# Optimization experiments

Hardware: AMD Instinct MI355X
Metric: run time of the kernel (lower is better)

The kernel has to match this reference:

```python
import jax, jax.numpy as jnp
import numpy as np

TOPK = 32  # init kwarg topk=32, method='softmax'


def setup_inputs() -> dict:
    key = jax.random.key(0)
    k1, k2 = jax.random.split(key)
    X1 = jax.random.normal(k1, (8192, 64), dtype=jnp.float32)
    X2 = jax.random.normal(k2, (8192, 64), dtype=jnp.float32)
    return {"X1": X1, "X2": X2}


def reference(X1, X2):
    # pairwise Euclidean distance via the matmul expansion (same math as torch.cdist p=2)
    sq = (
        jnp.sum(X1 * X1, axis=-1)[:, None]
        + jnp.sum(X2 * X2, axis=-1)[None, :]
        - 2.0 * (X1 @ X2.T)
    )  # [N1, N2]
    neg_dist = -jnp.sqrt(jnp.maximum(sq, 0.0))
    # top-k along dim=1, softmax over the k selected values
    val, idx = jax.lax.top_k(neg_dist, TOPK)          # [N1, K]
    score = jax.nn.softmax(val, axis=1)               # [N1, K]
    # scatter scores back into a dense zero matrix
    rows = jnp.arange(neg_dist.shape[0])[:, None]     # [N1, 1]
    out = jnp.zeros_like(neg_dist).at[rows, idx].set(score)
    return out, score
```

## Files before the change

### kernel.cpp

```cpp
#include <hip/hip_runtime.h>
#include <math.h>
#include <float.h>
#include <limits.h>

#define N 8192
#define D 64
#define TOPK 32
#define TILE 128
#define CAP 1024
#define CAP2 256
#define MARGIN 1.0f

typedef _Float16 f16x8 __attribute__((ext_vector_type(8)));
typedef _Float16 f16x4v __attribute__((ext_vector_type(4)));
typedef __attribute__((ext_vector_type(4))) float f32x4;

__device__ __forceinline__ unsigned ford(float f) {
    unsigned u = __float_as_uint(f);
    return u ^ ((u & 0x80000000u) ? 0xFFFFFFFFu : 0x80000000u);
}
__device__ __forceinline__ float finv(unsigned u) {
    unsigned b = (u & 0x80000000u) ? (u ^ 0x80000000u) : ~u;
    return __uint_as_float(b);
}

__global__ __launch_bounds__(256) void prep_kernel(
    const float* __restrict__ X1, const float* __restrict__ X2,
    float* __restrict__ nrm,
    _Float16* __restrict__ X1f, _Float16* __restrict__ X2f)
{
    int id = blockIdx.x * blockDim.x + threadIdx.x;
    if (id >= 2 * N) return;
    const float* X = (id < N) ? X1 : X2;
    _Float16* H = (id < N) ? X1f : X2f;
    int r = (id < N) ? id : id - N;
    const float4* p = (const float4*)(X + (size_t)r * D);
    f16x4v* ph = (f16x4v*)(H + (size_t)r * D);
    float s = 0.f;
#pragma unroll
    for (int q = 0; q < D / 4; ++q) {
        float4 v = p[q];
        s += v.x * v.x + v.y * v.y + v.z * v.z + v.w * v.w;
        f16x4v h;
        h[0] = (_Float16)v.x; h[1] = (_Float16)v.y;
        h[2] = (_Float16)v.z; h[3] = (_Float16)v.w;
        ph[q] = h;
    }
    nrm[id] = s;
}

#define MFMA16F(a, b, c) __builtin_amdgcn_mfma_f32_16x16x32_f16((a), (b), (c), 0, 0, 0)

__device__ __forceinline__ void stage_tile(
    const _Float16* __restrict__ gsrc, _Float16* __restrict__ lds, int t)
{
    const f16x8* g = (const f16x8*)gsrc;
#pragma unroll
    for (int it = 0; it < 4; ++it) {
        int idx = it * 256 + t;
        int row = idx >> 3;
        int co  = (idx & 7) << 3;
        int sw  = co ^ ((row & 7) << 3);
        *(f16x8*)&lds[row * 64 + sw] = g[idx];
    }
}

__device__ __forceinline__ void mfma_core_lds(
    const _Float16* __restrict__ Asm, const _Float16* __restrict__ Bsm,
    int wr, int wc, int lane, f32x4 acc[4][4])
{
    const int l15 = lane & 15;
    const int lg8 = (lane >> 4) * 8;

    f16x8 ah[4][2];
#pragma unroll
    for (int mt = 0; mt < 4; ++mt) {
        int row = wr * 64 + mt * 16 + l15;
        int sw0 = (lg8)      ^ ((row & 7) << 3);
        int sw1 = (32 + lg8) ^ ((row & 7) << 3);
        ah[mt][0] = *(const f16x8*)&Asm[row * 64 + sw0];
        ah[mt][1] = *(const f16x8*)&Asm[row * 64 + sw1];
    }
#pragma unroll
    for (int nt = 0; nt < 4; ++nt) {
        int row = wc * 64 + nt * 16 + l15;
        int sw0 = (lg8)      ^ ((row & 7) << 3);
        int sw1 = (32 + lg8) ^ ((row & 7) << 3);
        f16x8 b0 = *(const f16x8*)&Bsm[row * 64 + sw0];
        f16x8 b1 = *(const f16x8*)&Bsm[row * 64 + sw1];
#pragma unroll
        for (int mt = 0; mt < 4; ++mt) {
            acc[mt][nt] = MFMA16F(ah[mt][0], b0, acc[mt][nt]);
            acc[mt][nt] = MFMA16F(ah[mt][1], b1, acc[mt][nt]);
        }
    }
}

__global__ __launch_bounds__(256) void mfma_sz_kernel(
    const _Float16* __restrict__ X1f, const _Float16* __restrict__ X2f,
    const float* __restrict__ nrm, _Float16* __restrict__ S,
    float* __restrict__ tmax, float* __restrict__ out)
{
    __shared__ _Float16 smem[TILE * TILE];
    __shared__ float red[128][2];

    _Float16* Asm = smem;
    _Float16* Bsm = smem + TILE * D;

    const int t = threadIdx.x;
    const int lane = t & 63, w = t >> 6;
    const int wr = w >> 1, wc = w & 1;
    const int row0 = blockIdx.y * TILE, col0 = blockIdx.x * TILE;
    const int l15 = lane & 15, lg = lane >> 4;

    stage_tile(X1f + (size_t)row0 * D, Asm, t);
    stage_tile(X2f + (size_t)col0 * D, Bsm, t);

    const float4 zz = make_float4(0.f, 0.f, 0.f, 0.f);
#pragma unroll
    for (int p = 0; p < 16; ++p) {
        int lin = p * 256 + t;
        int rr = lin >> 5;
        int c4 = (lin & 31) << 2;
        *(float4*)(out + (size_t)(row0 + rr) * N + col0 + c4) = zz;
    }
    __syncthreads();

    f32x4 acc[4][4];
#pragma unroll
    for (int mt = 0; mt < 4; ++mt)
#pragma unroll
        for (int nt = 0; nt < 4; ++nt)
            acc[mt][nt] = (f32x4){0.f, 0.f, 0.f, 0.f};

    mfma_core_lds(Asm, Bsm, wr, wc, lane, acc);

    float nb[4];
#pragma unroll
    for (int nt = 0; nt < 4; ++nt) nb[nt] = nrm[N + col0 + wc * 64 + nt * 16 + l15];

    __syncthreads();

    float rmax[4][4];
#pragma unroll
    for (int mt = 0; mt < 4; ++mt) {
#pragma unroll
        for (int reg = 0; reg < 4; ++reg) {
            int lrow = wr * 64 + mt * 16 + lg * 4 + reg;
            float na = nrm[row0 + lrow];
            float rm = -FLT_MAX;
#pragma unroll
            for (int nt = 0; nt < 4; ++nt) {
                float v = -fmaxf(na + nb[nt] - 2.0f * acc[mt][nt][reg], 0.f);
                _Float16 h = (_Float16)v;
                smem[lrow * TILE + wc * 64 + nt * 16 + l15] = h;
                rm = fmaxf(rm, (float)h);
            }
            rmax[mt][reg] = rm;
        }
    }
    __syncthreads();

#pragma unroll
    for (int it = 0; it < 8; ++it) {
        int idx = it * 256 + t;
        int row = idx >> 4;
        int c8  = (idx & 15) << 3;
        *(f16x8*)(S + (size_t)(row0 + row) * N + col0 + c8) =
            *(const f16x8*)&smem[row * TILE + c8];
    }

#pragma unroll
    for (int off = 1; off < 16; off <<= 1)
#pragma unroll
        for (int mt = 0; mt < 4; ++mt)
#pragma unroll
            for (int reg = 0; reg < 4; ++reg)
                rmax[mt][reg] = fmaxf(rmax[mt][reg], __shfl_xor(rmax[mt][reg], off));

    if (l15 == 0) {
#pragma unroll
        for (int mt = 0; mt < 4; ++mt)
#pragma unroll
            for (int reg = 0; reg < 4; ++reg)
                red[wr * 64 + mt * 16 + lg * 4 + reg][wc] = rmax[mt][reg];
    }
    __syncthreads();
    if (t < 128)
        tmax[(size_t)(row0 + t) * 64 + blockIdx.x] = fmaxf(red[t][0], red[t][1]);
}

__global__ __launch_bounds__(256) void fused_topk_kernel(
    const float* __restrict__ X1, const float* __restrict__ X2,
    const float* __restrict__ nrm, const float* __restrict__ tmax,
    const _Float16* __restrict__ S, float* __restrict__ out,
    float* __restrict__ score_out)
{
    __shared__ float x1r[4][D];
    __shared__ float stm[4][64];
    __shared__ unsigned short lst[4][CAP2];
    __shared__ unsigned long long kl[4][CAP2];
    __shared__ int scnt[4];

    const int t = threadIdx.x;
    const int w = t >> 6;
    const int lane = t & 63;
    const int r = blockIdx.x * 4 + w;

    x1r[w][lane] = X1[(size_t)r * D + lane];
    float tm = tmax[(size_t)r * 64 + lane];
    stm[w][lane] = tm;
    if (lane == 0) scnt[w] = 0;

    unsigned km = ford(tm);
    int rk = 0;
#pragma unroll
    for (int l = 0; l < 64; ++l) {
        unsigned o = __shfl(km, l);
        rk += (o > km || (o == km && l < lane)) ? 1 : 0;
    }
    unsigned long long bm = __ballot(rk == 31);
    const float th = __shfl(tm, __ffsll(bm) - 1) - MARGIN;

    __builtin_amdgcn_s_waitcnt(0xC07F);

    const _Float16* Sr = S + (size_t)r * N;
    for (int c = 0; c < 16; ++c) {
        int st = c * 4 + (lane >> 4);
        if (stm[w][st] >= th) {
            f16x8 h8 = *(const f16x8*)(Sr + (size_t)(c * 64 + lane) * 8);
#pragma unroll
            for (int q = 0; q < 8; ++q) {
                float v = (float)h8[q];
                if (v >= th) {
                    int p = atomicAdd(&scnt[w], 1);
                    if (p < CAP2)
                        lst[w][p] = (unsigned short)((c * 64 + lane) * 8 + q);
                }
            }
        }
    }
    __builtin_amdgcn_s_waitcnt(0xC07F);
    const int n = min(scnt[w], CAP2);

    float na = nrm[r];
    for (int q = lane; q < n; q += 64) {
        int col = lst[w][q];
        const float4* xr = (const float4*)(X2 + (size_t)col * D);
        float dot = 0.f;
#pragma unroll
        for (int i = 0; i < D / 4; ++i) {
            float4 xv = xr[i];
            dot += x1r[w][4 * i + 0] * xv.x + x1r[w][4 * i + 1] * xv.y
                 + x1r[w][4 * i + 2] * xv.z + x1r[w][4 * i + 3] * xv.w;
        }
        float v = -fmaxf(na + nrm[N + col] - 2.0f * dot, 0.f);
        kl[w][q] = ((unsigned long long)ford(v) << 32) | (unsigned)(8191 - col);
    }
    __builtin_amdgcn_s_waitcnt(0xC07F);

    unsigned long long mykey = 0ull;
    for (int it = 0; it < TOPK; ++it) {
        unsigned long long b = 0ull; int bp = 0;
        for (int q = lane; q < n; q += 64) {
            unsigned long long kk = kl[w][q];
            if (kk > b) { b = kk; bp = q; }
        }
        for (int off = 32; off > 0; off >>= 1) {
            unsigned long long ob = __shfl_down(b, off);
            int op = __shfl_down(bp, off);
            if (ob > b) { b = ob; bp = op; }
        }
        unsigned long long b0 = __shfl(b, 0);
        int bp0 = __shfl(bp, 0);
        if (lane == it) { mykey = b0; kl[w][bp0] = 0ull; }
    }

    float myv = 0.f; int myj = 0;
    if (lane < TOPK) {
        float sv = finv((unsigned)(mykey >> 32));
        myv = -sqrtf(-sv);
        myj = 8191 - (int)(mykey & 0xFFFFFFFFu);
    }
    float Mx = __shfl(myv, 0);
    float e = (lane < TOPK) ? expf(myv - Mx) : 0.f;
    float Z = e;
    for (int off = 32; off > 0; off >>= 1) Z += __shfl_xor(Z, off);
    float s = e / Z;
    if (lane < TOPK) {
        score_out[(size_t)r * TOPK + lane] = s;
        out[(size_t)r * N + myj] = s;
    }
}

__global__ __launch_bounds__(256) void norms_kernel(
    const float* __restrict__ X1, const float* __restrict__ X2,
    float* __restrict__ nrm)
{
    int id = blockIdx.x * blockDim.x + threadIdx.x;
    if (id >= 2 * N) return;
    const float* X = (id < N) ? X1 : X2;
    int r = (id < N) ? id : id - N;
    const float4* p = (const float4*)(X + (size_t)r * D);
    float s = 0.f;
#pragma unroll
    for (int q = 0; q < D / 4; ++q) {
        float4 v = p[q];
        s += v.x * v.x + v.y * v.y + v.z * v.z + v.w * v.w;
    }
    nrm[id] = s;
}

__global__ __launch_bounds__(256, 2) void dist_kernel(
    const float* __restrict__ X1, const float* __restrict__ X2,
    const float* __restrict__ nrm, float* __restrict__ out,
    float* __restrict__ tmax, int have_tmax)
{
    __shared__ float As[D * TILE];
    __shared__ float Bs[D * TILE];

    const int t = threadIdx.x;
    const int row0 = blockIdx.y * TILE;
    const int col0 = blockIdx.x * TILE;

#pragma unroll
    for (int p = 0; p < 8; ++p) {
        int lin = p * 256 + t;
        int r   = lin >> 4;
        int d4  = (lin & 15) << 2;
        int g   = (d4 >> 2) & 7;
        int cb  = r ^ (g << 3);
        float4 a = *(const float4*)(X1 + (size_t)(row0 + r) * D + d4);
        As[(d4 + 0) * TILE + cb] = a.x;
        As[(d4 + 1) * TILE + cb] = a.y;
        As[(d4 + 2) * TILE + cb] = a.z;
        As[(d4 + 3) * TILE + cb] = a.w;
        float4 b = *(const float4*)(X2 + (size_t)(col0 + r) * D + d4);
        Bs[(d4 + 0) * TILE + cb] = b.x;
        Bs[(d4 + 1) * TILE + cb] = b.y;
        Bs[(d4 + 2) * TILE + cb] = b.z;
        Bs[(d4 + 3) * TILE + cb] = b.w;
    }
    __syncthreads();

    const int tx = t & 15;
    const int ty = t >> 4;
    float acc[8][8] = {};

#pragma unroll 8
    for (int k = 0; k < D; ++k) {
        int gk  = (k >> 2) & 7;
        int ab  = k * TILE + ((ty ^ gk) << 3);
        int bb0 = k * TILE + ((4 * tx) ^ (gk << 3));
        float4 a0 = *(const float4*)&As[ab];
        float4 a1 = *(const float4*)&As[ab + 4];
        float4 b0 = *(const float4*)&Bs[bb0];
        float4 b1 = *(const float4*)&Bs[bb0 + 64];
        float av[8] = {a0.x, a0.y, a0.z, a0.w, a1.x, a1.y, a1.z, a1.w};
        float bv[8] = {b0.x, b0.y, b0.z, b0.w, b1.x, b1.y, b1.z, b1.w};
#pragma unroll
        for (int i = 0; i < 8; ++i)
#pragma unroll
            for (int j = 0; j < 8; ++j)
                acc[i][j] += av[i] * bv[j];
    }

    float na[8], nb[8];
#pragma unroll
    for (int i = 0; i < 8; ++i) na[i] = nrm[row0 + 8 * ty + i];
#pragma unroll
    for (int q = 0; q < 4; ++q) {
        nb[q]     = nrm[N + col0 + 4 * tx + q];
        nb[4 + q] = nrm[N + col0 + 64 + 4 * tx + q];
    }

    float rmax[8];
#pragma unroll
    for (int i = 0; i < 8; ++i) rmax[i] = -FLT_MAX;

#pragma unroll
    for (int i = 0; i < 8; ++i) {
        float* po = out + (size_t)(row0 + 8 * ty + i) * N + col0 + 4 * tx;
        float4 o0, o1;
        float* f0 = (float*)&o0;
        float* f1 = (float*)&o1;
#pragma unroll
        for (int q = 0; q < 4; ++q) {
            float s0 = na[i] + nb[q] - 2.0f * acc[i][q];
            f0[q] = -fmaxf(s0, 0.0f);
            float s1 = na[i] + nb[4 + q] - 2.0f * acc[i][4 + q];
            f1[q] = -fmaxf(s1, 0.0f);
            rmax[i] = fmaxf(rmax[i], fmaxf(f0[q], f1[q]));
        }
        *(float4*)po        = o0;
        *(float4*)(po + 64) = o1;
    }

    if (have_tmax) {
#pragma unroll
        for (int i = 0; i < 8; ++i) {
            float mv = rmax[i];
            mv = fmaxf(mv, __shfl_down(mv, 8, 16));
            mv = fmaxf(mv, __shfl_down(mv, 4, 16));
            mv = fmaxf(mv, __shfl_down(mv, 2, 16));
            mv = fmaxf(mv, __shfl_down(mv, 1, 16));
            if (tx == 0)
                tmax[(size_t)(row0 + 8 * ty + i) * 64 + blockIdx.x] = mv;
        }
    }
}

__global__ __launch_bounds__(256) void topk_kernel(
    float* __restrict__ out, float* __restrict__ score_out,
    const float* __restrict__ tmax, int have_tmax)
{
    __shared__ unsigned long long candl[4][CAP];
    __shared__ int scnt[4];

    const int t    = threadIdx.x;
    const int w    = t >> 6;
    const int lane = t & 63;
    const int r    = blockIdx.x * 4 + w;
    float* row = out + (size_t)r * N;
    const float4* row4 = (const float4*)row;

    float thr;
    float lm = -FLT_MAX;
    if (have_tmax) {
        float tm = tmax[(size_t)r * 64 + lane];
        unsigned km = ford(tm);
        int rk = 0;
#pragma unroll
        for (int l = 0; l < 64; ++l) {
            unsigned o = __shfl(km, l);
            rk += (o > km || (o == km && l < lane)) ? 1 : 0;
        }
        unsigned long long bm = __ballot(rk == 31);
        thr = __shfl(tm, __ffsll(bm) - 1);
    } else {
#pragma unroll 8
        for (int c = 0; c < 32; ++c) {
            float4 x = row4[c * 64 + lane];
            lm = fmaxf(lm, fmaxf(fmaxf(x.x, x.y), fmaxf(x.z, x.w)));
        }
        thr = lm;
        for (int off = 32; off > 0; off >>= 1)
            thr = fminf(thr, __shfl_xor(thr, off));
    }

    for (int attempt = 0; ; ++attempt) {
        if (lane == 0) scnt[w] = 0;
        __builtin_amdgcn_s_waitcnt(0xC07F);
        for (int c = 0; c < 32; ++c) {
            float4 x = row4[c * 64 + lane];
            float vs[4] = {x.x, x.y, x.z, x.w};
#pragma unroll
            for (int q = 0; q < 4; ++q) {
                float v = vs[q];
                lm = fmaxf(lm, v);
                if (v >= thr) {
                    int p = atomicAdd(&scnt[w], 1);
                    if (p < CAP) {
                        unsigned long long key =
                            ((unsigned long long)ford(v) << 32) |
                            (unsigned)(8191 - (4 * (c * 64 + lane) + q));
                        candl[w][p] = key;
                    }
                }
            }
        }
        __builtin_amdgcn_s_waitcnt(0xC07F);
        if (scnt[w] <= CAP || attempt == 1) break;
        unsigned kml = ford(lm);
        int rk2 = 0;
#pragma unroll
        for (int l = 0; l < 64; ++l) {
            unsigned o = __shfl(kml, l);
            rk2 += (o < kml || (o == kml && l < lane)) ? 1 : 0;
        }
        unsigned long long bm2 = __ballot(rk2 == 15);
        float t2 = __shfl(lm, __ffsll(bm2) - 1);
        thr = fmaxf(thr, t2);
    }
    const int n = min(scnt[w], CAP);

    unsigned long long mykey = 0ull;
    for (int it = 0; it < TOPK; ++it) {
        unsigned long long b = 0ull; int bp = 0;
        for (int q = lane; q < n; q += 64) {
            unsigned long long kk = candl[w][q];
            if (kk > b) { b = kk; bp = q; }
        }
        for (int off = 32; off > 0; off >>= 1) {
            unsigned long long ob = __shfl_down(b, off);
            int op = __shfl_down(bp, off);
            if (ob > b) { b = ob; bp = op; }
        }
        unsigned long long b0 = __shfl(b, 0);
        int bp0 = __shfl(bp, 0);
        if (lane == it) { mykey = b0; candl[w][bp0] = 0ull; }
    }

    float myv = 0.f; int myj = 0;
    if (lane < TOPK) {
        float sv = finv((unsigned)(mykey >> 32));
        myv = -sqrtf(-sv);
        myj = 8191 - (int)(mykey & 0xFFFFFFFFu);
    }
    float Mx = __shfl(myv, 0);
    float e = (lane < TOPK) ? expf(myv - Mx) : 0.f;
    float Z = e;
    for (int off = 32; off > 0; off >>= 1) Z += __shfl_xor(Z, off);
    float s = e / Z;
    if (lane < TOPK) score_out[(size_t)r * TOPK + lane] = s;

    const float4 zz = make_float4(0.f, 0.f, 0.f, 0.f);
#pragma unroll 8
    for (int c = 0; c < 32; ++c) ((float4*)row)[c * 64 + lane] = zz;
    __builtin_amdgcn_s_waitcnt(0x0F70);
    if (lane < TOPK) row[myj] = s;
}

extern "C" void kernel_launch(void* const* d_in, const int* in_sizes, int n_in,
                              void* d_out, int out_size, void* d_ws, size_t ws_size,
                              hipStream_t stream)
{
    const float* X1 = (const float*)d_in[0];
    const float* X2 = (const float*)d_in[1];
    float* out = (float*)d_out;
    float* score = out + (size_t)N * N;

    char* base = (char*)d_ws;
    float* nrm  = (float*)base;
    float* tmax = nrm + 2 * N;
    _Float16* X1f = (_Float16*)(tmax + (size_t)N * 64);
    _Float16* X2f = X1f + (size_t)N * D;
    _Float16* S   = X2f + (size_t)N * D;

    size_t need_new = (size_t)(2 * N + (size_t)N * 64) * sizeof(float)
                    + 2 * (size_t)N * D * sizeof(_Float16)
                    + (size_t)N * N * sizeof(_Float16);
    size_t need_old = (size_t)(2 * N + (size_t)N * 64) * sizeof(float);

    if (ws_size >= need_new) {
        prep_kernel<<<(2 * N + 255) / 256, 256, 0, stream>>>(X1, X2, nrm, X1f, X2f);
        dim3 grid(N / TILE, N / TILE);
        mfma_sz_kernel<<<grid, 256, 0, stream>>>(X1f, X2f, nrm, S, tmax, out);
        fused_topk_kernel<<<N / 4, 256, 0, stream>>>(
            X1, X2, nrm, tmax, S, out, score);
    } else {
        float* tmax_f = nrm + 2 * N;
        int have_tmax = (ws_size >= need_old) ? 1 : 0;
        norms_kernel<<<(2 * N + 255) / 256, 256, 0, stream>>>(X1, X2, nrm);
        dim3 grid(N / TILE, N / TILE);
        dist_kernel<<<grid, 256, 0, stream>>>(X1, X2, nrm, out, tmax_f, have_tmax);
        topk_kernel<<<N / 4, 256, 0, stream>>>(out, score, tmax_f, have_tmax);
    }
}
```

Before: 443.9 us.

## Quantize screening distance matrix to uint8 and swizzle tile order

The intermediate negative squared-distance screening matrix is stored as 8-bit rounded integers instead of fp16. This halves the bytes written by the MFMA kernel and read back by the top-k candidate scan. To absorb the coarser quantization, the candidate margin is widened and the candidate list capacity grows, which risks more exact-recompute work per row. The MFMA tile launch order is also remapped with a block swizzle, intended to improve cache locality.

```diff
diff --git a/kernel.cpp b/kernel.cpp
--- a/kernel.cpp
+++ b/kernel.cpp
@@ -8,8 +8,8 @@
 #define TOPK 32
 #define TILE 128
 #define CAP 1024
-#define CAP2 256
-#define MARGIN 1.0f
+#define CAP2 384
+#define MARGIN 2.0f
 
 typedef _Float16 f16x8 __attribute__((ext_vector_type(8)));
 typedef _Float16 f16x4v __attribute__((ext_vector_type(4)));
@@ -22,6 +22,10 @@
 __device__ __forceinline__ float finv(unsigned u) {
     unsigned b = (u & 0x80000000u) ? (u ^ 0x80000000u) : ~u;
     return __uint_as_float(b);
+}
+__device__ __forceinline__ int quant_u8(float hneg) {
+    int q = (int)(-hneg + 0.5f);
+    return q > 255 ? 255 : q;
 }
 
 __global__ __launch_bounds__(256) void prep_kernel(
@@ -98,7 +102,7 @@
 
 __global__ __launch_bounds__(256) void mfma_sz_kernel(
     const _Float16* __restrict__ X1f, const _Float16* __restrict__ X2f,
-    const float* __restrict__ nrm, _Float16* __restrict__ S,
+    const float* __restrict__ nrm, unsigned char* __restrict__ S,
     float* __restrict__ tmax, float* __restrict__ out)
 {
     __shared__ _Float16 smem[TILE * TILE];
@@ -110,7 +114,9 @@
     const int t = threadIdx.x;
     const int lane = t & 63, w = t >> 6;
     const int wr = w >> 1, wc = w & 1;
-    const int row0 = blockIdx.y * TILE, col0 = blockIdx.x * TILE;
+    int flat = blockIdx.y * 64 + blockIdx.x;
+    int swz  = (flat & 7) * 512 + (flat >> 3);
+    const int row0 = (swz >> 6) * TILE, col0 = (swz & 63) * TILE;
     const int l15 = lane & 15, lg = lane >> 4;
 
     stage_tile(X1f + (size_t)row0 * D, Asm, t);
@@ -154,7 +160,7 @@
                 float v = -fmaxf(na + nb[nt] - 2.0f * acc[mt][nt][reg], 0.f);
                 _Float16 h = (_Float16)v;
                 smem[lrow * TILE + wc * 64 + nt * 16 + l15] = h;
-                rm = fmaxf(rm, (float)h);
+                rm = fmaxf(rm, -(float)quant_u8((float)h));
             }
             rmax[mt][reg] = rm;
         }
@@ -162,12 +168,20 @@
     __syncthreads();
 
 #pragma unroll
-    for (int it = 0; it < 8; ++it) {
+    for (int it = 0; it < 4; ++it) {
         int idx = it * 256 + t;
-        int row = idx >> 4;
-        int c8  = (idx & 15) << 3;
-        *(f16x8*)(S + (size_t)(row0 + row) * N + col0 + c8) =
-            *(const f16x8*)&smem[row * TILE + c8];
+        int row = idx >> 3;
+        int c16 = (idx & 7) << 4;
+        f16x8 h0 = *(const f16x8*)&smem[row * TILE + c16];
+        f16x8 h1 = *(const f16x8*)&smem[row * TILE + c16 + 8];
+        unsigned int wd[4] = {0u, 0u, 0u, 0u};
+#pragma unroll
+        for (int b = 0; b < 8; ++b) {
+            wd[b >> 2]     |= ((unsigned)quant_u8((float)h0[b])) << (8 * (b & 3));
+            wd[2 + (b >> 2)] |= ((unsigned)quant_u8((float)h1[b])) << (8 * (b & 3));
+        }
+        *(uint4*)(S + (size_t)(row0 + row) * N + col0 + c16) =
+            make_uint4(wd[0], wd[1], wd[2], wd[3]);
     }
 
 #pragma unroll
@@ -187,13 +201,13 @@
     }
     __syncthreads();
     if (t < 128)
-        tmax[(size_t)(row0 + t) * 64 + blockIdx.x] = fmaxf(red[t][0], red[t][1]);
+        tmax[(size_t)(row0 + t) * 64 + (swz & 63)] = fmaxf(red[t][0], red[t][1]);
 }
 
 __global__ __launch_bounds__(256) void fused_topk_kernel(
     const float* __restrict__ X1, const float* __restrict__ X2,
     const float* __restrict__ nrm, const float* __restrict__ tmax,
-    const _Float16* __restrict__ S, float* __restrict__ out,
+    const unsigned char* __restrict__ S, float* __restrict__ out,
     float* __restrict__ score_out)
 {
     __shared__ float x1r[4][D];
@@ -224,18 +238,23 @@
 
     __builtin_amdgcn_s_waitcnt(0xC07F);
 
-    const _Float16* Sr = S + (size_t)r * N;
-    for (int c = 0; c < 16; ++c) {
-        int st = c * 4 + (lane >> 4);
+    const unsigned char* Sr = S + (size_t)r * N;
+    for (int c = 0; c < 8; ++c) {
+        int chunk = c * 64 + lane;
+        int st = chunk >> 3;
         if (stm[w][st] >= th) {
-            f16x8 h8 = *(const f16x8*)(Sr + (size_t)(c * 64 + lane) * 8);
-#pragma unroll
-            for (int q = 0; q < 8; ++q) {
-                float v = (float)h8[q];
-                if (v >= th) {
-                    int p = atomicAdd(&scnt[w], 1);
-                    if (p < CAP2)
-                        lst[w][p] = (unsigned short)((c * 64 + lane) * 8 + q);
+            uint4 u = *(const uint4*)(Sr + (size_t)chunk * 16);
+            unsigned int ws[4] = {u.x, u.y, u.z, u.w};
+#pragma unroll
+            for (int g = 0; g < 4; ++g) {
+#pragma unroll
+                for (int b = 0; b < 4; ++b) {
+                    float v = -(float)((ws[g] >> (8 * b)) & 255u);
+                    if (v >= th) {
+                        int p = atomicAdd(&scnt[w], 1);
+                        if (p < CAP2)
+                            lst[w][p] = (unsigned short)(chunk * 16 + g * 4 + b);
+                    }
                 }
             }
         }
@@ -535,11 +554,11 @@
     float* tmax = nrm + 2 * N;
     _Float16* X1f = (_Float16*)(tmax + (size_t)N * 64);
     _Float16* X2f = X1f + (size_t)N * D;
-    _Float16* S   = X2f + (size_t)N * D;
+    unsigned char* S = (unsigned char*)(X2f + (size_t)N * D);
 
     size_t need_new = (size_t)(2 * N + (size_t)N * 64) * sizeof(float)
                     + 2 * (size_t)N * D * sizeof(_Float16)
-                    + (size_t)N * N * sizeof(_Float16);
+                    + (size_t)N * N * sizeof(unsigned char);
     size_t need_old = (size_t)(2 * N + (size_t)N * 64) * sizeof(float);
 
     if (ws_size >= need_new) {
```

Result: faster. 431.8 us (-2.7%).
